# Kernel tuning notes

Hardware: AMD Instinct MI355X
Metric: run time of the kernel (lower is better)

## Reference

```python
import jax, jax.numpy as jnp
import numpy as np

N, D, H, E, K = 16384, 1024, 4096, 8, 2
EPS = 1e-5


def setup_inputs() -> dict:
    key = jax.random.key(0)
    ks = jax.random.split(key, 12)
    s = 0.02
    return {
        "x": jax.random.normal(ks[0], (N, D), dtype=jnp.float32),
        "ln_g": jnp.ones((D,), jnp.float32),
        "ln_b": jnp.zeros((D,), jnp.float32),
        "r_w1": jax.random.normal(ks[1], (D, H // 2), jnp.float32) * s,
        "r_b1": jnp.zeros((H // 2,), jnp.float32),
        "r_w2": jax.random.normal(ks[2], (H // 2, E), jnp.float32) * s,
        "r_b2": jnp.zeros((E,), jnp.float32),
        "e_w1": jax.random.normal(ks[3], (E, D, H), jnp.float32) * s,
        "e_b1": jnp.zeros((E, H), jnp.float32),
        "e_w2": jax.random.normal(ks[4], (E, H, D), jnp.float32) * s,
        "e_b2": jnp.zeros((E, D), jnp.float32),
    }


def reference(x, ln_g, ln_b, r_w1, r_b1, r_w2, r_b2, e_w1, e_b1, e_w2, e_b2):
    # LayerNorm
    mu = jnp.mean(x, axis=-1, keepdims=True)
    var = jnp.mean(jnp.square(x - mu), axis=-1, keepdims=True)
    xn = (x - mu) * jax.lax.rsqrt(var + EPS) * ln_g + ln_b  # [N, D]

    # Router: Linear -> ReLU -> Linear -> softmax -> top-k, renormalize
    logits = jax.nn.relu(xn @ r_w1 + r_b1) @ r_w2 + r_b2  # [N, E]
    probs = jax.nn.softmax(logits, axis=-1)
    vals, idx = jax.lax.top_k(probs, K)  # [N, K]
    vals = vals / jnp.sum(vals, axis=-1, keepdims=True)

    # Dense expert dispatch: loop over fixed small E, weight by combine gate
    out = jnp.zeros_like(x)
    for e in range(E):
        gate = jnp.sum(vals * (idx == e).astype(vals.dtype), axis=-1)  # [N]
        h = jax.nn.relu(xn @ e_w1[e] + e_b1[e])  # dropout in eval mode -> identity
        y = h @ e_w2[e] + e_b2[e]  # [N, D]
        out = out + gate[:, None] * y
    return x + out
```

## Files before the change

### kernel.cpp

```cpp
#include <hip/hip_runtime.h>
#include <cstdint>
#include <cstddef>

typedef unsigned short u16;
typedef __attribute__((ext_vector_type(8))) short bf16x8;
typedef __attribute__((ext_vector_type(4))) float f32x4;

#define N_TOK 16384
#define DIM   1024
#define HID   4096
#define NEXP  8
#define HR    2048
#define TAU   0.02f
#define MAXMT 264

__device__ __forceinline__ u16 f2bf(float f) {
  union { float f; uint32_t u; } x; x.f = f;
  uint32_t r = x.u + 0x7FFFu + ((x.u >> 16) & 1u);
  return (u16)(r >> 16);
}
__device__ __forceinline__ float bf2f(u16 u) {
  union { uint32_t u; float f; } x; x.u = ((uint32_t)u) << 16; return x.f;
}

__device__ __forceinline__ void async16(const void* g, const void* l) {
  auto gp = reinterpret_cast<const __attribute__((address_space(1))) uint32_t*>(
      reinterpret_cast<uintptr_t>(g));
  auto lp = reinterpret_cast<__attribute__((address_space(3))) uint32_t*>(
      reinterpret_cast<uintptr_t>(l));
  __builtin_amdgcn_global_load_lds(gp, lp, 16, 0, 0);
}

__device__ __forceinline__ unsigned xcd_swz(unsigned flat, unsigned nwg) {
  const unsigned xcd = flat & 7u, lid = flat >> 3;
  const unsigned q = nwg >> 3, r = nwg & 7u;
  return (xcd < r ? xcd * (q + 1u) : r * (q + 1u) + (xcd - r) * q) + lid;
}

template<bool SPLIT>
__global__ __launch_bounds__(256)
void transpose_cvt(const float* __restrict__ src, u16* __restrict__ hi,
                   u16* __restrict__ lo, int R, int C)
{
  __shared__ float tile[32][33];
  const size_t bofs = (size_t)blockIdx.z * R * C;
  src += bofs; hi += bofs; if (SPLIT) lo += bofs;
  const int tx = threadIdx.x, ty = threadIdx.y;
  const int c0 = blockIdx.x * 32, r0 = blockIdx.y * 32;
#pragma unroll
  for (int i = 0; i < 4; ++i)
    tile[ty + i * 8][tx] = src[(size_t)(r0 + ty + i * 8) * C + c0 + tx];
  __syncthreads();
#pragma unroll
  for (int i = 0; i < 4; ++i) {
    float v = tile[tx][ty + i * 8];
    size_t o = (size_t)(c0 + ty + i * 8) * R + r0 + tx;
    u16 h = f2bf(v);
    hi[o] = h;
    if (SPLIT) lo[o] = f2bf(v - bf2f(h));
  }
}

__global__ __launch_bounds__(256)
void ln_kernel(const float* __restrict__ x, const float* __restrict__ g,
               const float* __restrict__ b, u16* __restrict__ xh,
               u16* __restrict__ xl, float* __restrict__ out)
{
  const int row = blockIdx.x;
  const int t = threadIdx.x;
  const float4 xv = ((const float4*)(x + (size_t)row * DIM))[t];
  float s = xv.x + xv.y + xv.z + xv.w;
  float q = xv.x * xv.x + xv.y * xv.y + xv.z * xv.z + xv.w * xv.w;
#pragma unroll
  for (int off = 32; off; off >>= 1) {
    s += __shfl_down(s, off, 64);
    q += __shfl_down(q, off, 64);
  }
  __shared__ float sm[8];
  __shared__ float mu_s, rs_s;
  const int lane = t & 63, wv = t >> 6;
  if (lane == 0) { sm[wv] = s; sm[wv + 4] = q; }
  __syncthreads();
  if (t == 0) {
    float S = sm[0] + sm[1] + sm[2] + sm[3];
    float Q = sm[4] + sm[5] + sm[6] + sm[7];
    float mu = S * (1.f / DIM);
    float var = Q * (1.f / DIM) - mu * mu;
    mu_s = mu; rs_s = rsqrtf(var + 1e-5f);
  }
  __syncthreads();
  const float mu = mu_s, rs = rs_s;
  const float4 gv = ((const float4*)g)[t];
  const float4 bv = ((const float4*)b)[t];
  float n0 = (xv.x - mu) * rs * gv.x + bv.x;
  float n1 = (xv.y - mu) * rs * gv.y + bv.y;
  float n2 = (xv.z - mu) * rs * gv.z + bv.z;
  float n3 = (xv.w - mu) * rs * gv.w + bv.w;
  ushort4 h, l;
  h.x = f2bf(n0); l.x = f2bf(n0 - bf2f(h.x));
  h.y = f2bf(n1); l.y = f2bf(n1 - bf2f(h.y));
  h.z = f2bf(n2); l.z = f2bf(n2 - bf2f(h.z));
  h.w = f2bf(n3); l.w = f2bf(n3 - bf2f(h.w));
  ((ushort4*)(xh + (size_t)row * DIM))[t] = h;
  ((ushort4*)(xl + (size_t)row * DIM))[t] = l;
  ((float4*)(out + (size_t)row * DIM))[t] = xv;
}

__global__ __launch_bounds__(256)
void logits_kernel(const u16* __restrict__ HrB, const float* __restrict__ w2,
                   float* __restrict__ logits)
{
  const int row = blockIdx.x, t = threadIdx.x;
  const u16* h = HrB + (size_t)row * HR;
  const ushort4* hv = (const ushort4*)(h + t * 8);
  ushort4 h0 = hv[0], h1 = hv[1];
  u16 hh[8] = {h0.x, h0.y, h0.z, h0.w, h1.x, h1.y, h1.z, h1.w};
  float p[8] = {0, 0, 0, 0, 0, 0, 0, 0};
#pragma unroll
  for (int j = 0; j < 8; ++j) {
    const int col = t * 8 + j;
    const float v = bf2f(hh[j]);
    const float4* wp = (const float4*)(w2 + (size_t)col * 8);
    float4 a = wp[0], b = wp[1];
    p[0] += v * a.x; p[1] += v * a.y; p[2] += v * a.z; p[3] += v * a.w;
    p[4] += v * b.x; p[5] += v * b.y; p[6] += v * b.z; p[7] += v * b.w;
  }
#pragma unroll
  for (int off = 32; off; off >>= 1)
#pragma unroll
    for (int e = 0; e < 8; ++e) p[e] += __shfl_down(p[e], off, 64);
  __shared__ float sm[4][8];
  const int lane = t & 63, wv = t >> 6;
  if (lane == 0) {
#pragma unroll
    for (int e = 0; e < 8; ++e) sm[wv][e] = p[e];
  }
  __syncthreads();
  if (t < 8)
    logits[(size_t)row * 8 + t] = sm[0][t] + sm[1][t] + sm[2][t] + sm[3][t];
}

__device__ __forceinline__ void load_logits(const float* logits, const float* b2,
                                            int row, float l[8]) {
  const float4* lp = (const float4*)(logits + (size_t)row * 8);
  float4 a = lp[0], b = lp[1];
  l[0] = a.x + b2[0]; l[1] = a.y + b2[1]; l[2] = a.z + b2[2]; l[3] = a.w + b2[3];
  l[4] = b.x + b2[4]; l[5] = b.y + b2[5]; l[6] = b.z + b2[6]; l[7] = b.w + b2[7];
}
__device__ __forceinline__ void top2(const float l[8], int& i0, float& l0,
                                     int& i1, float& l1) {
  i0 = 0; l0 = l[0];
#pragma unroll
  for (int e = 1; e < 8; ++e) if (l[e] > l0) { l0 = l[e]; i0 = e; }
  i1 = -1; l1 = -1e30f;
#pragma unroll
  for (int e = 0; e < 8; ++e) if (e != i0 && l[e] > l1) { l1 = l[e]; i1 = e; }
}

__global__ __launch_bounds__(256)
void pass_flag(float* __restrict__ logits, const float* __restrict__ b2,
               int* __restrict__ fixL, int* __restrict__ cntFix)
{
  __shared__ int lcnt;
  __shared__ int base;
  const int t = threadIdx.x;
  const int row = blockIdx.x * 256 + t;
  if (t == 0) lcnt = 0;
  float l[8]; load_logits(logits, b2, row, l);
  int i0, i1; float l0, l1;
  top2(l, i0, l0, i1, l1);
  float l2 = -1e30f;
#pragma unroll
  for (int e = 0; e < 8; ++e)
    if (e != i0 && e != i1 && l[e] > l2) l2 = l[e];
  const bool flag = (l1 - l2) < TAU;
  __syncthreads();
  int r = 0;
  if (flag) r = atomicAdd(&lcnt, 1);
  __syncthreads();
  if (t == 0) base = atomicAdd(cntFix, lcnt);
  __syncthreads();
  if (flag) {
    fixL[base + r] = row;
    float4 z = {0.f, 0.f, 0.f, 0.f};
    ((float4*)(logits + (size_t)row * 8))[0] = z;
    ((float4*)(logits + (size_t)row * 8))[1] = z;
  }
}

__global__ __launch_bounds__(256)
void pass_count(const float* __restrict__ logits, const float* __restrict__ b2,
                int* __restrict__ cnts)
{
  __shared__ int lcnt[NEXP];
  const int t = threadIdx.x;
  const int row = blockIdx.x * 256 + t;
  if (t < NEXP) lcnt[t] = 0;
  float l[8]; load_logits(logits, b2, row, l);
  int i0, i1; float l0, l1;
  top2(l, i0, l0, i1, l1);
  __syncthreads();
  atomicAdd(&lcnt[i0], 1);
  atomicAdd(&lcnt[i1], 1);
  __syncthreads();
  if (t < NEXP) atomicAdd(&cnts[t], lcnt[t]);
}

__global__ void scan_kernel(const int* __restrict__ cnts, int* __restrict__ offs,
                            int* __restrict__ tileOffs)
{
  if (threadIdx.x == 0) {
    int s = 0, ts = 0;
#pragma unroll
    for (int e = 0; e < NEXP; ++e) {
      offs[e] = s; s += cnts[e];
      tileOffs[e] = ts; ts += (cnts[e] + 127) >> 7;
    }
    offs[NEXP] = s;
    tileOffs[NEXP] = ts;
  }
}

__global__ __launch_bounds__(256)
void pass_scatter(const float* __restrict__ logits, const float* __restrict__ b2,
                  const int* __restrict__ offs, int* __restrict__ cnts2,
                  int* __restrict__ rowsC, float* __restrict__ gateC)
{
  __shared__ int lcnt[NEXP];
  __shared__ int sbase[NEXP];
  const int t = threadIdx.x;
  const int row = blockIdx.x * 256 + t;
  if (t < NEXP) lcnt[t] = 0;
  float l[8]; load_logits(logits, b2, row, l);
  int i0, i1; float l0, l1;
  top2(l, i0, l0, i1, l1);
  float tt = expf(l1 - l0);
  float g0 = 1.f / (1.f + tt);
  float g1 = tt / (1.f + tt);
  __syncthreads();
  int r0 = atomicAdd(&lcnt[i0], 1);
  int r1 = atomicAdd(&lcnt[i1], 1);
  __syncthreads();
  if (t < NEXP) sbase[t] = atomicAdd(&cnts2[t], lcnt[t]);
  __syncthreads();
  int p0 = offs[i0] + sbase[i0] + r0;
  int p1 = offs[i1] + sbase[i1] + r1;
  rowsC[p0] = row; gateC[p0] = g0;
  rowsC[p1] = row; gateC[p1] = g1;
}

template<bool SPLIT, int EPI, bool GATHER, bool FUSED>
__global__ __launch_bounds__(256, 2)
void gemm_bt(const u16* __restrict__ A0, const u16* __restrict__ A1,
             const u16* __restrict__ B0, const u16* __restrict__ B1,
             int lda, int ldb, int K, int M,
             size_t bStrideE, int biasStrideE,
             const int* __restrict__ counts, int expertArg,
             const int* __restrict__ offs, const int* __restrict__ tileOffs,
             const int* __restrict__ rowsC, const float* __restrict__ gatesC,
             const float* __restrict__ bias,
             const float* __restrict__ w2, float* __restrict__ logits,
             u16* __restrict__ Cbf, float* __restrict__ Cf32, int ldc)
{
  int expert, m0, n0;
  if constexpr (FUSED) {
    const int NT = expertArg;
    const unsigned swz = xcd_swz(blockIdx.x, gridDim.x);
    const int mt = (int)(swz / (unsigned)NT);
    if (mt >= tileOffs[NEXP]) return;
    int e = 0;
#pragma unroll
    for (int i = 1; i < NEXP; ++i) if (tileOffs[i] <= mt) e = i;
    expert = e;
    m0 = (mt - tileOffs[e]) * 128;
    n0 = (int)(swz % (unsigned)NT) * 128;
  } else if (counts == nullptr) {
    const unsigned nwg = gridDim.x * gridDim.y;
    const unsigned flat = blockIdx.y * gridDim.x + blockIdx.x;
    const unsigned swz = xcd_swz(flat, nwg);
    expert = expertArg;
    m0 = (int)(swz / gridDim.x) * 128;
    n0 = (int)(swz % gridDim.x) * 128;
  } else {
    expert = expertArg;
    m0 = blockIdx.y * 128;
    n0 = blockIdx.x * 128;
  }

  const int Mq = counts ? counts[expert] : M;
  if (m0 >= Mq) return;
  const int off = offs ? offs[expert] : 0;
  const int* rows = rowsC ? rowsC + off : nullptr;
  const float* gates = gatesC ? gatesC + off : nullptr;
  const u16* B = B0 + (FUSED ? (size_t)expert * bStrideE : 0);
  const u16* Bl = SPLIT ? B1 : nullptr;
  const float* bi = bias + (FUSED ? (size_t)expert * biasStrideE : 0);
  const int z = FUSED ? 0 : (int)blockIdx.z;
  const int zOff = z * K;

  __shared__ u16 As0[128 * 32], Bs0[128 * 32];
  __shared__ u16 As1[SPLIT ? 128 * 32 : 8], Bs1[SPLIT ? 128 * 32 : 8];

  const int t = threadIdx.x;
  size_t aoff[2]; int acodd[2]; size_t boff[2];
#pragma unroll
  for (int i = 0; i < 2; ++i) {
    int gdx = i * 256 + t;
    int ar = gdx >> 2, ac = (gdx & 3) * 8;
    int am = m0 + ar;
    int amc = am < Mq ? am : (Mq - 1);
    int agr = GATHER ? rows[amc] : amc;
    if (FUSED && EPI == 2) agr += off;
    aoff[i] = (size_t)agr * lda + ac + zOff;
    boff[i] = (size_t)(n0 + ar) * ldb + ac + zOff;
    acodd[i] = gdx * 8;
  }

  f32x4 acc[4][4];
#pragma unroll
  for (int i = 0; i < 4; ++i)
#pragma unroll
    for (int j = 0; j < 4; ++j) acc[i][j] = (f32x4){0.f, 0.f, 0.f, 0.f};

  const int lane = t & 63, wv = t >> 6;
  const int wm = (wv >> 1) * 64, wn = (wv & 1) * 64;
  const int fr = lane & 15, fq = lane >> 4;

  for (int k0 = 0; k0 < K; k0 += 32) {
    __syncthreads();
#pragma unroll
    for (int i = 0; i < 2; ++i) {
      async16(A0 + aoff[i] + k0, &As0[acodd[i]]);
      async16(B + boff[i] + k0, &Bs0[acodd[i]]);
      if (SPLIT) {
        async16(A1 + aoff[i] + k0, &As1[acodd[i]]);
        async16(Bl + boff[i] + k0, &Bs1[acodd[i]]);
      }
    }
    __syncthreads();
    bf16x8 af[4], bfr[4], af1[4], bf1[4];
#pragma unroll
    for (int xi = 0; xi < 4; ++xi) {
      af[xi]  = *(const bf16x8*)&As0[(wm + xi * 16 + fr) * 32 + fq * 8];
      bfr[xi] = *(const bf16x8*)&Bs0[(wn + xi * 16 + fr) * 32 + fq * 8];
      if (SPLIT) {
        af1[xi] = *(const bf16x8*)&As1[(wm + xi * 16 + fr) * 32 + fq * 8];
        bf1[xi] = *(const bf16x8*)&Bs1[(wn + xi * 16 + fr) * 32 + fq * 8];
      }
    }
#pragma unroll
    for (int mt = 0; mt < 4; ++mt)
#pragma unroll
      for (int nt = 0; nt < 4; ++nt) {
        acc[mt][nt] = __builtin_amdgcn_mfma_f32_16x16x32_bf16(af[mt], bfr[nt], acc[mt][nt], 0, 0, 0);
        if (SPLIT) {
          acc[mt][nt] = __builtin_amdgcn_mfma_f32_16x16x32_bf16(af[mt], bf1[nt], acc[mt][nt], 0, 0, 0);
          acc[mt][nt] = __builtin_amdgcn_mfma_f32_16x16x32_bf16(af1[mt], bfr[nt], acc[mt][nt], 0, 0, 0);
        }
      }
  }

  if constexpr (EPI == 3) {
    float w2v[4][8]; float b1v[4];
#pragma unroll
    for (int nt = 0; nt < 4; ++nt) {
      const int n = n0 + wn + nt * 16 + fr;
      b1v[nt] = bi[n];
      const float4* wp = (const float4*)(w2 + (size_t)n * 8);
      float4 wa = wp[0], wb = wp[1];
      w2v[nt][0] = wa.x; w2v[nt][1] = wa.y; w2v[nt][2] = wa.z; w2v[nt][3] = wa.w;
      w2v[nt][4] = wb.x; w2v[nt][5] = wb.y; w2v[nt][6] = wb.z; w2v[nt][7] = wb.w;
    }
#pragma unroll
    for (int mt = 0; mt < 4; ++mt) {
      float pe[4][8];
#pragma unroll
      for (int r = 0; r < 4; ++r)
#pragma unroll
        for (int e = 0; e < 8; ++e) pe[r][e] = 0.f;
#pragma unroll
      for (int nt = 0; nt < 4; ++nt)
#pragma unroll
        for (int r = 0; r < 4; ++r) {
          float v = fmaxf(acc[mt][nt][r] + b1v[nt], 0.f);
#pragma unroll
          for (int e = 0; e < 8; ++e) pe[r][e] += v * w2v[nt][e];
        }
#pragma unroll
      for (int offx = 1; offx < 16; offx <<= 1)
#pragma unroll
        for (int r = 0; r < 4; ++r)
#pragma unroll
          for (int e = 0; e < 8; ++e)
            pe[r][e] += __shfl_xor(pe[r][e], offx, 64);
      if (fr == 0) {
#pragma unroll
        for (int r = 0; r < 4; ++r) {
          const int m = m0 + wm + mt * 16 + fq * 4 + r;
          if (m < Mq) {
            const int lrow = GATHER ? rows[m] : m;
#pragma unroll
            for (int e = 0; e < 8; ++e)
              atomicAdd(&logits[(size_t)lrow * 8 + e], pe[r][e]);
          }
        }
      }
    }
    return;
  }

#pragma unroll
  for (int mt = 0; mt < 4; ++mt) {
#pragma unroll
    for (int nt = 0; nt < 4; ++nt) {
      const int n = n0 + wn + nt * 16 + fr;
      const float bv = (z == 0) ? bi[n] : 0.f;
#pragma unroll
      for (int r = 0; r < 4; ++r) {
        const int m = m0 + wm + mt * 16 + fq * 4 + r;
        if (m < Mq) {
          float v = acc[mt][nt][r] + bv;
          if constexpr (EPI == 1) {
            const int crow = m + (FUSED ? off : 0);
            Cbf[(size_t)crow * ldc + n] = f2bf(fmaxf(v, 0.f));
          } else {
            atomicAdd(&Cf32[(size_t)rows[m] * ldc + n], gates[m] * v);
          }
        }
      }
    }
  }
}

extern "C" void kernel_launch(void* const* d_in, const int* in_sizes, int n_in,
                              void* d_out, int out_size, void* d_ws, size_t ws_size,
                              hipStream_t stream)
{
  const float* x    = (const float*)d_in[0];
  const float* ln_g = (const float*)d_in[1];
  const float* ln_b = (const float*)d_in[2];
  const float* r_w1 = (const float*)d_in[3];
  const float* r_b1 = (const float*)d_in[4];
  const float* r_w2 = (const float*)d_in[5];
  const float* r_b2 = (const float*)d_in[6];
  const float* e_w1 = (const float*)d_in[7];
  const float* e_b1 = (const float*)d_in[8];
  const float* e_w2 = (const float*)d_in[9];
  const float* e_b2 = (const float*)d_in[10];
  float* out = (float*)d_out;

  char* ws = (char*)d_ws;
  const size_t MB = 1024ull * 1024ull;
  u16*   xnhi = (u16*)(ws);
  u16*   xnlo = (u16*)(ws + 32 * MB);
  u16*   rw1h = (u16*)(ws + 64 * MB);
  u16*   rw1l = (u16*)(ws + 68 * MB);
  u16*   ew1t = (u16*)(ws + 72 * MB);
  u16*   ew2t = (u16*)(ws + 136 * MB);
  float* logits = (float*)(ws + 200 * MB);
  int*   rowsC  = (int*)(ws + 200 * MB + 512 * 1024);
  float* gateC  = (float*)(ws + 200 * MB + 640 * 1024);
  int*   fixL   = (int*)(ws + 200 * MB + 768 * 1024);
  int*   cntb   = (int*)(ws + 200 * MB + 832 * 1024);
  int*   cnts   = cntb;
  int*   cnts2  = cntb + 8;
  int*   offs   = cntb + 16;
  int*   cntFix = cntb + 25;
  int*   tileOffs = cntb + 32;
  u16*   Hbuf = (u16*)(ws + 201 * MB);
  u16*   HrB  = Hbuf;
  (void)in_sizes; (void)n_in; (void)out_size;

  const bool fused = ws_size >= 458ull * MB;

  hipMemsetAsync(cntb, 0, 256, stream);

  dim3 tb(32, 8);
  transpose_cvt<true ><<<dim3(HR / 32, DIM / 32, 1), tb, 0, stream>>>(r_w1, rw1h, rw1l, DIM, HR);
  transpose_cvt<false><<<dim3(HID / 32, DIM / 32, NEXP), tb, 0, stream>>>(e_w1, ew1t, nullptr, DIM, HID);
  transpose_cvt<false><<<dim3(DIM / 32, HID / 32, NEXP), tb, 0, stream>>>(e_w2, ew2t, nullptr, HID, DIM);

  ln_kernel<<<N_TOK, 256, 0, stream>>>(x, ln_g, ln_b, xnhi, xnlo, out);

  gemm_bt<false, 1, false, false><<<dim3(HR / 128, N_TOK / 128), 256, 0, stream>>>(
      xnhi, nullptr, rw1h, nullptr, DIM, DIM, DIM, N_TOK, 0, 0,
      nullptr, 0, nullptr, nullptr, nullptr, nullptr, r_b1, nullptr, nullptr,
      HrB, nullptr, HR);

  logits_kernel<<<N_TOK, 256, 0, stream>>>(HrB, r_w2, logits);

  pass_flag<<<N_TOK / 256, 256, 0, stream>>>(logits, r_b2, fixL, cntFix);

  gemm_bt<true, 3, true, false><<<dim3(HR / 128, N_TOK / 128), 256, 0, stream>>>(
      xnhi, xnlo, rw1h, rw1l, DIM, DIM, DIM, N_TOK, 0, 0,
      cntFix, 0, nullptr, nullptr, fixL, nullptr, r_b1, r_w2, logits,
      nullptr, nullptr, 0);

  pass_count<<<N_TOK / 256, 256, 0, stream>>>(logits, r_b2, cnts);
  scan_kernel<<<1, 64, 0, stream>>>(cnts, offs, tileOffs);
  pass_scatter<<<N_TOK / 256, 256, 0, stream>>>(logits, r_b2, offs, cnts2, rowsC, gateC);

  if (fused) {
    gemm_bt<false, 1, true, true><<<dim3((HID / 128) * MAXMT), 256, 0, stream>>>(
        xnhi, nullptr, ew1t, nullptr, DIM, DIM, DIM, N_TOK,
        (size_t)HID * DIM, HID,
        cnts, HID / 128, offs, tileOffs, rowsC, nullptr, e_b1, nullptr, nullptr,
        Hbuf, nullptr, HID);
    gemm_bt<false, 2, false, true><<<dim3((DIM / 128) * MAXMT), 256, 0, stream>>>(
        Hbuf, nullptr, ew2t, nullptr, HID, HID, HID, N_TOK,
        (size_t)DIM * HID, DIM,
        cnts, DIM / 128, offs, tileOffs, rowsC, gateC, e_b2, nullptr, nullptr,
        nullptr, out, DIM);
  } else {
    for (int e = 0; e < NEXP; ++e) {
      gemm_bt<false, 1, true, false><<<dim3(HID / 128, N_TOK / 128), 256, 0, stream>>>(
          xnhi, nullptr, ew1t + (size_t)e * HID * DIM, nullptr,
          DIM, DIM, DIM, N_TOK, 0, 0,
          cnts, e, offs, nullptr, rowsC, nullptr, e_b1 + (size_t)e * HID, nullptr, nullptr,
          Hbuf, nullptr, HID);
      gemm_bt<false, 2, false, false><<<dim3(DIM / 128, N_TOK / 128, 2), 256, 0, stream>>>(
          Hbuf, nullptr, ew2t + (size_t)e * DIM * HID, nullptr,
          HID, HID, HID / 2, N_TOK, 0, 0,
          cnts, e, offs, nullptr, rowsC, gateC, e_b2 + (size_t)e * DIM, nullptr, nullptr,
          nullptr, out, DIM);
    }
  }
}
```

Measured before the change: 1.578 ms.

## Add dedicated pipelined MoE expert GEMM with 128x256 tiles and async LDS loads

Replaces the fused expert GEMM path with a new gemm_moe kernel. It uses 512 threads per block, 128x256 output tiles, swizzled LDS layouts and a multi-stage asynchronous global-to-LDS pipeline (8-deep for A, 4-deep for B) with explicit vmcnt waits and priority raises around the MFMA block. The aim is to hide memory latency and raise arithmetic intensity in the two dominant expert GEMMs. It uses much more LDS per block, which may lower occupancy, and the wider tiles waste more work on partially filled per-expert tiles.

```diff
diff --git a/kernel.cpp b/kernel.cpp
--- a/kernel.cpp
+++ b/kernel.cpp
@@ -249,32 +249,163 @@
   rowsC[p1] = row; gateC[p1] = g1;
 }
 
-template<bool SPLIT, int EPI, bool GATHER, bool FUSED>
+template<int EPI, bool GATHER>
+__global__ __launch_bounds__(512, 2)
+void gemm_moe(const u16* __restrict__ A0, const u16* __restrict__ B0,
+              int lda, int ldb, int K, int NT,
+              size_t bStrideE, int biasStrideE,
+              const int* __restrict__ counts,
+              const int* __restrict__ offs, const int* __restrict__ tileOffs,
+              const int* __restrict__ rowsC, const float* __restrict__ gatesC,
+              const float* __restrict__ bias,
+              u16* __restrict__ Cbf, float* __restrict__ Cf32, int ldc)
+{
+  const unsigned swz = xcd_swz(blockIdx.x, gridDim.x);
+  const int mt = (int)(swz / (unsigned)NT);
+  if (mt >= tileOffs[NEXP]) return;
+  int e = 0;
+#pragma unroll
+  for (int i = 1; i < NEXP; ++i) if (tileOffs[i] <= mt) e = i;
+  const int m0 = (mt - tileOffs[e]) * 128;
+  const int n0 = (int)(swz % (unsigned)NT) * 256;
+  const int Mq = counts[e];
+  if (m0 >= Mq) return;
+
+  const int off = offs[e];
+  const int* rows = rowsC + off;
+  const u16* B = B0 + (size_t)e * bStrideE;
+  const float* bi = bias + (size_t)e * biasStrideE;
+
+  __shared__ alignas(16) u16 As[8][128 * 32];
+  __shared__ alignas(16) u16 Bs[4][256 * 32];
+
+  const int t = threadIdx.x;
+  const int numK = K >> 5;
+
+  const int rloc = t >> 2;
+  const int cb = ((t & 3) << 4) ^ (((t >> 5) & 1) << 5);
+  const int csrc = cb >> 1;
+  const int arow0 = m0 + rloc;
+  const int amc = arow0 < Mq ? arow0 : (Mq - 1);
+  const size_t agr = GATHER ? (size_t)rows[amc] : (size_t)(off + amc);
+  const u16* aSrc = A0 + agr * lda + csrc;
+  const u16* bSrc0 = B + (size_t)(n0 + rloc) * ldb + csrc;
+  const u16* bSrc1 = B + (size_t)(n0 + 128 + rloc) * ldb + csrc;
+
+#pragma unroll
+  for (int h = 0; h < 6; ++h)
+    if (h < numK) async16(aSrc + h * 32, &As[h][t * 8]);
+#pragma unroll
+  for (int h = 0; h < 2; ++h)
+    if (h < numK) {
+      async16(bSrc0 + h * 32, &Bs[h][t * 8]);
+      async16(bSrc1 + h * 32, &Bs[h][4096 + t * 8]);
+    }
+  asm volatile("s_waitcnt vmcnt(2)" ::: "memory");
+  __builtin_amdgcn_s_barrier();
+  __builtin_amdgcn_sched_barrier(0);
+
+  const int lane = t & 63, wv = t >> 6;
+  const int wm = wv >> 2;
+  const int wn = wv & 3;
+  const int fr = lane & 15, fq = lane >> 4;
+
+  int aIdx[4], bIdx[4];
+#pragma unroll
+  for (int mf = 0; mf < 4; ++mf) {
+    const int r = wm * 64 + mf * 16 + fr;
+    aIdx[mf] = r * 32 + ((fq * 8) ^ (((r >> 3) & 1) << 4));
+  }
+#pragma unroll
+  for (int nf = 0; nf < 4; ++nf) {
+    const int rb = wn * 64 + nf * 16 + fr;
+    bIdx[nf] = rb * 32 + ((fq * 8) ^ (((rb >> 3) & 1) << 4));
+  }
+
+  f32x4 acc[4][4];
+#pragma unroll
+  for (int i = 0; i < 4; ++i)
+#pragma unroll
+    for (int j = 0; j < 4; ++j) acc[i][j] = (f32x4){0.f, 0.f, 0.f, 0.f};
+
+  for (int T = 0; T < numK; ++T) {
+    const u16* aLds = As[T & 7];
+    const u16* bLds = Bs[T & 3];
+    bf16x8 aF[4], bF[4];
+#pragma unroll
+    for (int i = 0; i < 4; ++i) {
+      aF[i] = *(const bf16x8*)&aLds[aIdx[i]];
+      bF[i] = *(const bf16x8*)&bLds[bIdx[i]];
+    }
+    const bool stA = (T + 6) < numK;
+    const bool stB = (T + 2) < numK;
+    if (stA) async16(aSrc + (T + 6) * 32, &As[(T + 6) & 7][t * 8]);
+    if (stB) {
+      async16(bSrc0 + (T + 2) * 32, &Bs[(T + 2) & 3][t * 8]);
+      async16(bSrc1 + (T + 2) * 32, &Bs[(T + 2) & 3][4096 + t * 8]);
+    }
+    __builtin_amdgcn_s_barrier();
+    __builtin_amdgcn_sched_barrier(0);
+    __builtin_amdgcn_s_setprio(1);
+#pragma unroll
+    for (int mf = 0; mf < 4; ++mf)
+#pragma unroll
+      for (int nf = 0; nf < 4; ++nf)
+        acc[mf][nf] = __builtin_amdgcn_mfma_f32_16x16x32_bf16(
+            aF[mf], bF[nf], acc[mf][nf], 0, 0, 0);
+    __builtin_amdgcn_s_setprio(0);
+    __builtin_amdgcn_sched_barrier(0);
+    if (stA && stB) asm volatile("s_waitcnt vmcnt(3)" ::: "memory");
+    else if (stB)   asm volatile("s_waitcnt vmcnt(2)" ::: "memory");
+    else            asm volatile("s_waitcnt vmcnt(0)" ::: "memory");
+    __builtin_amdgcn_s_barrier();
+    __builtin_amdgcn_sched_barrier(0);
+  }
+
+  float bv[4];
+#pragma unroll
+  for (int nf = 0; nf < 4; ++nf) bv[nf] = bi[n0 + wn * 64 + nf * 16 + fr];
+
+#pragma unroll
+  for (int mf = 0; mf < 4; ++mf)
+#pragma unroll
+    for (int r = 0; r < 4; ++r) {
+      const int m = m0 + wm * 64 + mf * 16 + fq * 4 + r;
+      if (m < Mq) {
+        if constexpr (EPI == 2) {
+          const size_t orow = (size_t)rows[m];
+          const float g = gatesC[off + m];
+#pragma unroll
+          for (int nf = 0; nf < 4; ++nf) {
+            const int n = n0 + wn * 64 + nf * 16 + fr;
+            atomicAdd(&Cf32[orow * ldc + n], g * (acc[mf][nf][r] + bv[nf]));
+          }
+        } else {
+#pragma unroll
+          for (int nf = 0; nf < 4; ++nf) {
+            const int n = n0 + wn * 64 + nf * 16 + fr;
+            Cbf[(size_t)(off + m) * ldc + n] =
+                f2bf(fmaxf(acc[mf][nf][r] + bv[nf], 0.f));
+          }
+        }
+      }
+    }
+}
+
+template<bool SPLIT, int EPI, bool GATHER>
 __global__ __launch_bounds__(256, 2)
 void gemm_bt(const u16* __restrict__ A0, const u16* __restrict__ A1,
              const u16* __restrict__ B0, const u16* __restrict__ B1,
              int lda, int ldb, int K, int M,
-             size_t bStrideE, int biasStrideE,
              const int* __restrict__ counts, int expertArg,
-             const int* __restrict__ offs, const int* __restrict__ tileOffs,
+             const int* __restrict__ offs,
              const int* __restrict__ rowsC, const float* __restrict__ gatesC,
              const float* __restrict__ bias,
              const float* __restrict__ w2, float* __restrict__ logits,
              u16* __restrict__ Cbf, float* __restrict__ Cf32, int ldc)
 {
   int expert, m0, n0;
-  if constexpr (FUSED) {
-    const int NT = expertArg;
-    const unsigned swz = xcd_swz(blockIdx.x, gridDim.x);
-    const int mt = (int)(swz / (unsigned)NT);
-    if (mt >= tileOffs[NEXP]) return;
-    int e = 0;
-#pragma unroll
-    for (int i = 1; i < NEXP; ++i) if (tileOffs[i] <= mt) e = i;
-    expert = e;
-    m0 = (mt - tileOffs[e]) * 128;
-    n0 = (int)(swz % (unsigned)NT) * 128;
-  } else if (counts == nullptr) {
+  if (counts == nullptr) {
     const unsigned nwg = gridDim.x * gridDim.y;
     const unsigned flat = blockIdx.y * gridDim.x + blockIdx.x;
     const unsigned swz = xcd_swz(flat, nwg);
@@ -292,10 +423,10 @@
   const int off = offs ? offs[expert] : 0;
   const int* rows = rowsC ? rowsC + off : nullptr;
   const float* gates = gatesC ? gatesC + off : nullptr;
-  const u16* B = B0 + (FUSED ? (size_t)expert * bStrideE : 0);
+  const u16* B = B0;
   const u16* Bl = SPLIT ? B1 : nullptr;
-  const float* bi = bias + (FUSED ? (size_t)expert * biasStrideE : 0);
-  const int z = FUSED ? 0 : (int)blockIdx.z;
+  const float* bi = bias;
+  const int z = (int)blockIdx.z;
   const int zOff = z * K;
 
   __shared__ u16 As0[128 * 32], Bs0[128 * 32];
@@ -310,7 +441,6 @@
     int am = m0 + ar;
     int amc = am < Mq ? am : (Mq - 1);
     int agr = GATHER ? rows[amc] : amc;
-    if (FUSED && EPI == 2) agr += off;
     aoff[i] = (size_t)agr * lda + ac + zOff;
     boff[i] = (size_t)(n0 + ar) * ldb + ac + zOff;
     acodd[i] = gdx * 8;
@@ -377,22 +507,22 @@
 #pragma unroll
       for (int r = 0; r < 4; ++r)
 #pragma unroll
-        for (int e = 0; e < 8; ++e) pe[r][e] = 0.f;
+        for (int ee = 0; ee < 8; ++ee) pe[r][ee] = 0.f;
 #pragma unroll
       for (int nt = 0; nt < 4; ++nt)
 #pragma unroll
         for (int r = 0; r < 4; ++r) {
           float v = fmaxf(acc[mt][nt][r] + b1v[nt], 0.f);
 #pragma unroll
-          for (int e = 0; e < 8; ++e) pe[r][e] += v * w2v[nt][e];
+          for (int ee = 0; ee < 8; ++ee) pe[r][ee] += v * w2v[nt][ee];
         }
 #pragma unroll
       for (int offx = 1; offx < 16; offx <<= 1)
 #pragma unroll
         for (int r = 0; r < 4; ++r)
 #pragma unroll
-          for (int e = 0; e < 8; ++e)
-            pe[r][e] += __shfl_xor(pe[r][e], offx, 64);
+          for (int ee = 0; ee < 8; ++ee)
+            pe[r][ee] += __shfl_xor(pe[r][ee], offx, 64);
       if (fr == 0) {
 #pragma unroll
         for (int r = 0; r < 4; ++r) {
@@ -400,8 +530,8 @@
           if (m < Mq) {
             const int lrow = GATHER ? rows[m] : m;
 #pragma unroll
-            for (int e = 0; e < 8; ++e)
-              atomicAdd(&logits[(size_t)lrow * 8 + e], pe[r][e]);
+            for (int ee = 0; ee < 8; ++ee)
+              atomicAdd(&logits[(size_t)lrow * 8 + ee], pe[r][ee]);
           }
         }
       }
@@ -414,15 +544,14 @@
 #pragma unroll
     for (int nt = 0; nt < 4; ++nt) {
       const int n = n0 + wn + nt * 16 + fr;
-      const float bv = (z == 0) ? bi[n] : 0.f;
+      const float bvv = (z == 0) ? bi[n] : 0.f;
 #pragma unroll
       for (int r = 0; r < 4; ++r) {
         const int m = m0 + wm + mt * 16 + fq * 4 + r;
         if (m < Mq) {
-          float v = acc[mt][nt][r] + bv;
+          float v = acc[mt][nt][r] + bvv;
           if constexpr (EPI == 1) {
-            const int crow = m + (FUSED ? off : 0);
-            Cbf[(size_t)crow * ldc + n] = f2bf(fmaxf(v, 0.f));
+            Cbf[(size_t)m * ldc + n] = f2bf(fmaxf(v, 0.f));
           } else {
             atomicAdd(&Cf32[(size_t)rows[m] * ldc + n], gates[m] * v);
           }
@@ -482,18 +611,18 @@
 
   ln_kernel<<<N_TOK, 256, 0, stream>>>(x, ln_g, ln_b, xnhi, xnlo, out);
 
-  gemm_bt<false, 1, false, false><<<dim3(HR / 128, N_TOK / 128), 256, 0, stream>>>(
-      xnhi, nullptr, rw1h, nullptr, DIM, DIM, DIM, N_TOK, 0, 0,
-      nullptr, 0, nullptr, nullptr, nullptr, nullptr, r_b1, nullptr, nullptr,
+  gemm_bt<false, 1, false><<<dim3(HR / 128, N_TOK / 128), 256, 0, stream>>>(
+      xnhi, nullptr, rw1h, nullptr, DIM, DIM, DIM, N_TOK,
+      nullptr, 0, nullptr, nullptr, nullptr, r_b1, nullptr, nullptr,
       HrB, nullptr, HR);
 
   logits_kernel<<<N_TOK, 256, 0, stream>>>(HrB, r_w2, logits);
 
   pass_flag<<<N_TOK / 256, 256, 0, stream>>>(logits, r_b2, fixL, cntFix);
 
-  gemm_bt<true, 3, true, false><<<dim3(HR / 128, N_TOK / 128), 256, 0, stream>>>(
-      xnhi, xnlo, rw1h, rw1l, DIM, DIM, DIM, N_TOK, 0, 0,
-      cntFix, 0, nullptr, nullptr, fixL, nullptr, r_b1, r_w2, logits,
+  gemm_bt<true, 3, true><<<dim3(HR / 128, N_TOK / 128), 256, 0, stream>>>(
+      xnhi, xnlo, rw1h, rw1l, DIM, DIM, DIM, N_TOK,
+      cntFix, 0, nullptr, fixL, nullptr, r_b1, r_w2, logits,
       nullptr, nullptr, 0);
 
   pass_count<<<N_TOK / 256, 256, 0, stream>>>(logits, r_b2, cnts);
@@ -501,27 +630,27 @@
   pass_scatter<<<N_TOK / 256, 256, 0, stream>>>(logits, r_b2, offs, cnts2, rowsC, gateC);
 
   if (fused) {
-    gemm_bt<false, 1, true, true><<<dim3((HID / 128) * MAXMT), 256, 0, stream>>>(
-        xnhi, nullptr, ew1t, nullptr, DIM, DIM, DIM, N_TOK,
+    gemm_moe<1, true><<<dim3((HID / 256) * MAXMT), 512, 0, stream>>>(
+        xnhi, ew1t, DIM, DIM, DIM, HID / 256,
         (size_t)HID * DIM, HID,
-        cnts, HID / 128, offs, tileOffs, rowsC, nullptr, e_b1, nullptr, nullptr,
+        cnts, offs, tileOffs, rowsC, nullptr, e_b1,
         Hbuf, nullptr, HID);
-    gemm_bt<false, 2, false, true><<<dim3((DIM / 128) * MAXMT), 256, 0, stream>>>(
-        Hbuf, nullptr, ew2t, nullptr, HID, HID, HID, N_TOK,
+    gemm_moe<2, false><<<dim3((DIM / 256) * MAXMT), 512, 0, stream>>>(
+        Hbuf, ew2t, HID, HID, HID, DIM / 256,
         (size_t)DIM * HID, DIM,
-        cnts, DIM / 128, offs, tileOffs, rowsC, gateC, e_b2, nullptr, nullptr,
+        cnts, offs, tileOffs, rowsC, gateC, e_b2,
         nullptr, out, DIM);
   } else {
     for (int e = 0; e < NEXP; ++e) {
-      gemm_bt<false, 1, true, false><<<dim3(HID / 128, N_TOK / 128), 256, 0, stream>>>(
+      gemm_bt<false, 1, true><<<dim3(HID / 128, N_TOK / 128), 256, 0, stream>>>(
           xnhi, nullptr, ew1t + (size_t)e * HID * DIM, nullptr,
-          DIM, DIM, DIM, N_TOK, 0, 0,
-          cnts, e, offs, nullptr, rowsC, nullptr, e_b1 + (size_t)e * HID, nullptr, nullptr,
+          DIM, DIM, DIM, N_TOK,
+          cnts, e, offs, rowsC, nullptr, e_b1 + (size_t)e * HID, nullptr, nullptr,
           Hbuf, nullptr, HID);
-      gemm_bt<false, 2, false, false><<<dim3(DIM / 128, N_TOK / 128, 2), 256, 0, stream>>>(
+      gemm_bt<false, 2, false><<<dim3(DIM / 128, N_TOK / 128, 2), 256, 0, stream>>>(
           Hbuf, nullptr, ew2t + (size_t)e * DIM * HID, nullptr,
-          HID, HID, HID / 2, N_TOK, 0, 0,
-          cnts, e, offs, nullptr, rowsC, gateC, e_b2 + (size_t)e * DIM, nullptr, nullptr,
+          HID, HID, HID / 2, N_TOK,
+          cnts, e, offs, rowsC, gateC, e_b2 + (size_t)e * DIM, nullptr, nullptr,
           nullptr, out, DIM);
     }
   }
```

Result: no change. 1.584 ms (+0.4%).
